# Kernel tuning notes

Hardware: AMD Instinct MI355X
Metric: run time of the kernel (lower is better)

## Reference

```python
import jax, jax.numpy as jnp
import numpy as np

DIM = 512
HEADS = 8
WIN = 10      # window_size
SHIFT = 5     # shift_size
FRAMES = 1000 # num_frames (N)
HIDDEN = 4 * DIM
EPS = 1e-5


def _layernorm(x, w, b):
    m = jnp.mean(x, axis=-1, keepdims=True)
    v = jnp.mean((x - m) ** 2, axis=-1, keepdims=True)
    return (x - m) * jax.lax.rsqrt(v + EPS) * w + b


def _shift_mask(N):
    pos = jnp.arange(N)
    seg = (pos >= N - WIN).astype(jnp.float32) + (pos >= N - SHIFT).astype(jnp.float32)
    seg = seg.reshape(N // WIN, WIN)
    diff = seg[:, :, None] - seg[:, None, :]
    return jnp.where(diff != 0, -100.0, 0.0)


def setup_inputs() -> dict:
    key = jax.random.key(0)
    ks = jax.random.split(key, 16)
    std = 0.02
    inp = {
        "x": jax.random.normal(ks[0], (64, FRAMES, DIM), dtype=jnp.float32),
        "norm1_w": jnp.ones((DIM,), jnp.float32),
        "norm1_b": jnp.zeros((DIM,), jnp.float32),
        "qkv_w": jax.random.normal(ks[1], (3 * DIM, DIM), jnp.float32) * std,
        "qkv_b": jnp.zeros((3 * DIM,), jnp.float32),
        "rel_bias_table": jax.random.normal(ks[2], (2 * WIN - 1, HEADS), jnp.float32) * std,
        "proj_w": jax.random.normal(ks[3], (DIM, DIM), jnp.float32) * std,
        "proj_b": jnp.zeros((DIM,), jnp.float32),
        "norm2_w": jnp.ones((DIM,), jnp.float32),
        "norm2_b": jnp.zeros((DIM,), jnp.float32),
        "fc1_w": jax.random.normal(ks[4], (HIDDEN, DIM), jnp.float32) * std,
        "fc1_b": jnp.zeros((HIDDEN,), jnp.float32),
        "fc2_w": jax.random.normal(ks[5], (DIM, HIDDEN), jnp.float32) * std,
        "fc2_b": jnp.zeros((DIM,), jnp.float32),
    }
    return inp


def reference(x, norm1_w, norm1_b, qkv_w, qkv_b, rel_bias_table, proj_w, proj_b,
              norm2_w, norm2_b, fc1_w, fc1_b, fc2_w, fc2_b):
    B, N, C = x.shape
    hd = C // HEADS
    scale = hd ** -0.5
    nW = N // WIN

    shortcut = x
    h = _layernorm(x, norm1_w, norm1_b)
    h = jnp.roll(h, -SHIFT, axis=1)                      # cyclic shift
    xw = h.reshape(B * nW, WIN, C)                       # window partition

    qkv = xw @ qkv_w.T + qkv_b
    qkv = qkv.reshape(B * nW, WIN, 3, HEADS, hd).transpose(2, 0, 3, 1, 4)
    q, k, v = qkv[0] * scale, qkv[1], qkv[2]

    attn = jnp.einsum('bhqd,bhkd->bhqk', q, k)
    idx = jnp.arange(WIN)[:, None] - jnp.arange(WIN)[None, :] + WIN - 1
    bias = rel_bias_table[idx]
    attn = attn + bias.transpose(2, 0, 1)[None]

    mask = _shift_mask(N)
    attn = attn.reshape(B, nW, HEADS, WIN, WIN) + mask[None, :, None]
    attn = jax.nn.softmax(attn, axis=-1).reshape(B * nW, HEADS, WIN, WIN)

    out = jnp.einsum('bhqk,bhkd->bhqd', attn, v)
    out = out.transpose(0, 2, 1, 3).reshape(B * nW, WIN, C)
    out = out @ proj_w.T + proj_b

    out = out.reshape(B, N, C)                           # window reverse
    out = jnp.roll(out, SHIFT, axis=1)                   # reverse shift

    x = shortcut + out
    h2 = _layernorm(x, norm2_w, norm2_b)
    h2 = jax.nn.gelu(h2 @ fc1_w.T + fc1_b, approximate=False)
    h2 = h2 @ fc2_w.T + fc2_b
    return x + h2
```

## Files before the change

### kernel.cpp

```cpp
#include <hip/hip_runtime.h>

#define DIMC 512
#define HEADS 8
#define HD 64
#define WINS 10
#define SHIFT_SZ 5
#define FRAMES 1000
#define NWIN 100
#define BATCH 64
#define TOKENS 64000
#define HIDDEN 2048

typedef unsigned short u16;
typedef __attribute__((ext_vector_type(8))) short bf16x8;
typedef __attribute__((ext_vector_type(4))) float f32x4;

__device__ __forceinline__ float bf2f(u16 u) { return __uint_as_float(((unsigned)u) << 16); }
__device__ __forceinline__ u16 f2bf(float f) {
    unsigned u = __float_as_uint(f);
    u += 0x7fffu + ((u >> 16) & 1u);
    return (u16)(u >> 16);
}

__global__ __launch_bounds__(256) void cvt_kernel(const float* __restrict__ src,
                                                  u16* __restrict__ dst, int n) {
    const int i = (blockIdx.x * 256 + threadIdx.x) * 4;
    if (i < n) {
        const float4 v = *(const float4*)(src + i);
        *(ushort4*)(dst + i) = make_ushort4(f2bf(v.x), f2bf(v.y), f2bf(v.z), f2bf(v.w));
    }
}

template <int SH>
__global__ __launch_bounds__(256) void ln_kernel(const float* __restrict__ x,
                                                 const float* __restrict__ w,
                                                 const float* __restrict__ b,
                                                 u16* __restrict__ out,
                                                 u16* __restrict__ xb) {
    const int wave = threadIdx.x >> 6, lane = threadIdx.x & 63;
    const int row = blockIdx.x * 4 + wave;
    const float4* rp = (const float4*)(x + (size_t)row * DIMC);
    const float4 v0 = rp[lane];
    const float4 v1 = rp[64 + lane];
    float f[8] = {v0.x, v0.y, v0.z, v0.w, v1.x, v1.y, v1.z, v1.w};
    float sum = 0.f, sq = 0.f;
#pragma unroll
    for (int i = 0; i < 8; i++) { sum += f[i]; sq += f[i] * f[i]; }
#pragma unroll
    for (int off = 32; off >= 1; off >>= 1) {
        sum += __shfl_xor(sum, off);
        sq += __shfl_xor(sq, off);
    }
    const float mean = sum * (1.f / DIMC);
    const float var = sq * (1.f / DIMC) - mean * mean;
    const float rstd = rsqrtf(var + 1e-5f);

    if (xb) {
        u16* xp = xb + (size_t)row * DIMC;
        *(ushort4*)(xp + 4 * lane) = make_ushort4(f2bf(f[0]), f2bf(f[1]), f2bf(f[2]), f2bf(f[3]));
        *(ushort4*)(xp + 256 + 4 * lane) = make_ushort4(f2bf(f[4]), f2bf(f[5]), f2bf(f[6]), f2bf(f[7]));
    }

    const float4 w0 = ((const float4*)w)[lane], w1 = ((const float4*)w)[64 + lane];
    const float4 b0 = ((const float4*)b)[lane], b1 = ((const float4*)b)[64 + lane];
    const float wf[8] = {w0.x, w0.y, w0.z, w0.w, w1.x, w1.y, w1.z, w1.w};
    const float bf[8] = {b0.x, b0.y, b0.z, b0.w, b1.x, b1.y, b1.z, b1.w};
    u16 o[8];
#pragma unroll
    for (int i = 0; i < 8; i++) o[i] = f2bf((f[i] - mean) * rstd * wf[i] + bf[i]);

    int dst = row;
    if (SH) {
        int bb = row / FRAMES;
        int t = row - bb * FRAMES;
        int td = t - SH; if (td < 0) td += FRAMES;
        dst = bb * FRAMES + td;
    }
    u16* op = out + (size_t)dst * DIMC;
    *(ushort4*)(op + 4 * lane) = make_ushort4(o[0], o[1], o[2], o[3]);
    *(ushort4*)(op + 256 + 4 * lane) = make_ushort4(o[4], o[5], o[6], o[7]);
}

__global__ __launch_bounds__(256) void ln_kernel_bf(const u16* __restrict__ x,
                                                    const float* __restrict__ w,
                                                    const float* __restrict__ b,
                                                    u16* __restrict__ out) {
    const int wave = threadIdx.x >> 6, lane = threadIdx.x & 63;
    const int row = blockIdx.x * 4 + wave;
    const uint4 v = ((const uint4*)(x + (size_t)row * DIMC))[lane];
    const unsigned uv[4] = {v.x, v.y, v.z, v.w};
    float f[8];
    float sum = 0.f, sq = 0.f;
#pragma unroll
    for (int i = 0; i < 4; i++) {
        float a = __uint_as_float(uv[i] << 16);
        float c = __uint_as_float(uv[i] & 0xffff0000u);
        f[2 * i] = a; f[2 * i + 1] = c;
        sum += a + c; sq += a * a + c * c;
    }
#pragma unroll
    for (int off = 32; off >= 1; off >>= 1) {
        sum += __shfl_xor(sum, off);
        sq += __shfl_xor(sq, off);
    }
    const float mean = sum * (1.f / DIMC);
    const float var = sq * (1.f / DIMC) - mean * mean;
    const float rstd = rsqrtf(var + 1e-5f);

    const float4 w0 = ((const float4*)w)[2 * lane], w1 = ((const float4*)w)[2 * lane + 1];
    const float4 b0 = ((const float4*)b)[2 * lane], b1 = ((const float4*)b)[2 * lane + 1];
    const float wf[8] = {w0.x, w0.y, w0.z, w0.w, w1.x, w1.y, w1.z, w1.w};
    const float bf[8] = {b0.x, b0.y, b0.z, b0.w, b1.x, b1.y, b1.z, b1.w};
    u16 o[8];
#pragma unroll
    for (int i = 0; i < 8; i++) o[i] = f2bf((f[i] - mean) * rstd * wf[i] + bf[i]);
    uint4 ov;
    ov.x = (unsigned)o[0] | ((unsigned)o[1] << 16);
    ov.y = (unsigned)o[2] | ((unsigned)o[3] << 16);
    ov.z = (unsigned)o[4] | ((unsigned)o[5] << 16);
    ov.w = (unsigned)o[6] | ((unsigned)o[7] << 16);
    ((uint4*)(out + (size_t)row * DIMC))[lane] = ov;
}

#define GLD16(gp, lp)                                                                     \
    __builtin_amdgcn_global_load_lds((const __attribute__((address_space(1))) void*)(gp), \
                                     (__attribute__((address_space(3))) void*)(lp), 16, 0, 0)

template <int MODE>
__global__ __launch_bounds__(256, 2) void gemm_bt(const u16* __restrict__ A,
                                                  const u16* __restrict__ W,
                                                  const float* __restrict__ bias,
                                                  u16* __restrict__ Cb,
                                                  float* __restrict__ Cf,
                                                  const u16* __restrict__ Rb,
                                                  int Nn, int K, int nbn) {
    __shared__ __align__(16) u16 smem[36864];
    const int tid = threadIdx.x;
    const int w = tid >> 6, l = tid & 63;

    const int nwg = gridDim.x;
    const int q8 = nwg >> 3, r8 = nwg & 7;
    const int xcd = blockIdx.x & 7, bidx = blockIdx.x >> 3;
    const int swz = (xcd < r8 ? xcd * (q8 + 1) : r8 * (q8 + 1) + (xcd - r8) * q8) + bidx;
    const int bm = swz / nbn, bn = swz - bm * nbn;

    const int wr = w >> 1, wc = w & 1;
    const int lrow = l & 15, lq = l >> 4;

    f32x4 acc[8][4];
#pragma unroll
    for (int m = 0; m < 8; m++)
#pragma unroll
        for (int n = 0; n < 4; n++) acc[m][n] = (f32x4)0.0f;

    const int gsrc8 = (((tid & 3) ^ ((tid >> 3) & 3)) << 3);
    const u16* Ag = A + (size_t)(bm * 256 + (tid >> 2)) * K + gsrc8;
    const u16* Bg = W + (size_t)(bn * 128 + (tid >> 2)) * K + gsrc8;
    const size_t rowoff = (size_t)64 * K;
    const int lb = w * 512;

#define STAGE(buf, kt) do {                                       \
        u16* sb_ = smem + (buf) * 12288;                          \
        GLD16(Ag + (kt), sb_ + lb);                               \
        GLD16(Ag + rowoff + (kt), sb_ + 2048 + lb);               \
        GLD16(Ag + 2 * rowoff + (kt), sb_ + 4096 + lb);           \
        GLD16(Ag + 3 * rowoff + (kt), sb_ + 6144 + lb);           \
        GLD16(Bg + (kt), sb_ + 8192 + lb);                        \
        GLD16(Bg + rowoff + (kt), sb_ + 10240 + lb);              \
    } while (0)

    const int gran = ((lq ^ ((lrow >> 1) & 3)) << 3);
    const int arow = (wr * 128 + lrow) * 32 + gran;
    const int brow = 8192 + (wc * 64 + lrow) * 32 + gran;

#define COMPUTE(buf) do {                                                          \
        const u16* sb = smem + (buf) * 12288;                                      \
        bf16x8 bv[4];                                                              \
        _Pragma("unroll")                                                          \
        for (int n = 0; n < 4; n++) bv[n] = *(const bf16x8*)(sb + brow + n * 512); \
        _Pragma("unroll")                                                          \
        for (int m = 0; m < 8; m++) {                                              \
            const bf16x8 af = *(const bf16x8*)(sb + arow + m * 512);               \
            _Pragma("unroll")                                                      \
            for (int n = 0; n < 4; n++)              \
                acc[m][n] = __builtin_amdgcn_mfma_f32_16x16x32_bf16(bv[n], af, acc[m][n], 0, 0, 0); \
        }                                                                          \
    } while (0)

    const int nt = K >> 5;
    STAGE(0, 0);
    STAGE(1, 32);
    int cb = 0;
    for (int t = 0; t < nt - 1; ++t) {
        asm volatile("s_waitcnt vmcnt(6)" ::: "memory");
        __builtin_amdgcn_s_barrier();
        __builtin_amdgcn_sched_barrier(0);
        COMPUTE(cb);
        if (t + 2 < nt) {
            const int sbuf = cb == 0 ? 2 : cb - 1;
            STAGE(sbuf, (t + 2) * 32);
        }
        cb = cb == 2 ? 0 : cb + 1;
    }
    asm volatile("s_waitcnt vmcnt(0)" ::: "memory");
    __builtin_amdgcn_s_barrier();
    __builtin_amdgcn_sched_barrier(0);
    COMPUTE(cb);

    if (MODE == 0 || MODE == 1 || MODE == 2) {
        __syncthreads();
#pragma unroll
        for (int m = 0; m < 8; m++) {
            const int row = wr * 128 + m * 16 + lrow;
            const int sw = (row & 7) << 3;
#pragma unroll
            for (int n = 0; n < 4; n++) {
                const int col = wc * 64 + n * 16 + lq * 4;
                const float4 b4 = *(const float4*)(bias + bn * 128 + col);
                float v0 = acc[m][n][0] + b4.x, v1 = acc[m][n][1] + b4.y;
                float v2 = acc[m][n][2] + b4.z, v3 = acc[m][n][3] + b4.w;
                if (MODE == 2) {
                    const float g0 = v0 * (0.7978845608f + 0.0356774081f * v0 * v0);
                    const float g1 = v1 * (0.7978845608f + 0.0356774081f * v1 * v1);
                    const float g2 = v2 * (0.7978845608f + 0.0356774081f * v2 * v2);
                    const float g3 = v3 * (0.7978845608f + 0.0356774081f * v3 * v3);
                    v0 /= (1.f + __expf(-2.f * g0)); v1 /= (1.f + __expf(-2.f * g1));
                    v2 /= (1.f + __expf(-2.f * g2)); v3 /= (1.f + __expf(-2.f * g3));
                }
                *(ushort4*)(smem + row * 128 + ((col ^ sw))) =
                    make_ushort4(f2bf(v0), f2bf(v1), f2bf(v2), f2bf(v3));
            }
        }
        __syncthreads();
        const int c8 = lrow * 8;
#pragma unroll
        for (int i = 0; i < 16; i++) {
            const int r = w * 64 + i * 4 + lq;
            const uint4 val = *(const uint4*)(smem + r * 128 + (c8 ^ ((r & 7) << 3)));
            const int grow = bm * 256 + r;
            if (MODE == 1) {
                int bb = grow / FRAMES;
                int tr = grow - bb * FRAMES;
                int td = tr + SHIFT_SZ; if (td >= FRAMES) td -= FRAMES;
                const size_t dr = (size_t)(bb * FRAMES + td) * DIMC + bn * 128 + c8;
                const uint4 rv = *(const uint4*)(Rb + dr);
                const u16* vp = (const u16*)&val;
                const u16* rp2 = (const u16*)&rv;
                u16 o[8];
#pragma unroll
                for (int k = 0; k < 8; k++) o[k] = f2bf(bf2f(vp[k]) + bf2f(rp2[k]));
                uint4 ov;
                ov.x = (unsigned)o[0] | ((unsigned)o[1] << 16);
                ov.y = (unsigned)o[2] | ((unsigned)o[3] << 16);
                ov.z = (unsigned)o[4] | ((unsigned)o[5] << 16);
                ov.w = (unsigned)o[6] | ((unsigned)o[7] << 16);
                *(uint4*)(Cb + dr) = ov;
            } else {
                *(uint4*)(Cb + (size_t)grow * Nn + bn * 128 + c8) = val;
            }
        }
    } else {
#pragma unroll
        for (int m = 0; m < 8; m++) {
            const int grow = bm * 256 + wr * 128 + m * 16 + lrow;
#pragma unroll
            for (int n = 0; n < 4; n++) {
                const int gcb = bn * 128 + wc * 64 + n * 16 + lq * 4;
                const float4 b4 = *(const float4*)(bias + gcb);
                const size_t dr = (size_t)grow * Nn + gcb;
                const ushort4 rb = *(const ushort4*)(Rb + dr);
                float4 o;
                o.x = acc[m][n][0] + b4.x + bf2f(rb.x);
                o.y = acc[m][n][1] + b4.y + bf2f(rb.y);
                o.z = acc[m][n][2] + b4.z + bf2f(rb.z);
                o.w = acc[m][n][3] + b4.w + bf2f(rb.w);
                *(float4*)(Cf + dr) = o;
            }
        }
    }
#undef COMPUTE
#undef STAGE
}

__global__ __launch_bounds__(256) void attn_kernel(const u16* __restrict__ qkv_c,
                                                   const float* __restrict__ relb,
                                                   u16* __restrict__ out,
                                                   int win0) {
    __shared__ __align__(16) u16 kv[WINS * 3 * DIMC];
    __shared__ float S[HEADS][WINS][WINS];
    const int tid = threadIdx.x;
    const int win = win0 + blockIdx.x;
    const u16* src = qkv_c + (size_t)blockIdx.x * (WINS * 3 * DIMC);
    for (int idx = tid * 8; idx < WINS * 3 * DIMC; idx += 2048)
        *(uint4*)(kv + idx) = *(const uint4*)(src + idx);
    __syncthreads();

    const bool lastw = (win % NWIN) == (NWIN - 1);
    for (int e = tid; e < HEADS * WINS * WINS; e += 256) {
        const int hh = e / (WINS * WINS);
        const int rem = e - hh * WINS * WINS;
        const int i = rem / WINS, j = rem - (rem / WINS) * WINS;
        const u16* qp = kv + i * (3 * DIMC) + hh * HD;
        const u16* kp = kv + j * (3 * DIMC) + DIMC + hh * HD;
        float s = 0.f;
#pragma unroll
        for (int c = 0; c < 64; c++) s += bf2f(qp[c]) * bf2f(kp[c]);
        s *= 0.125f;
        s += relb[(i - j + WINS - 1) * HEADS + hh];
        if (lastw && ((i < SHIFT_SZ) != (j < SHIFT_SZ))) s -= 100.f;
        S[hh][i][j] = s;
    }
    __syncthreads();

    if (tid < HEADS * WINS) {
        const int hh = tid / WINS, i = tid - (tid / WINS) * WINS;
        float m = -1e30f;
#pragma unroll
        for (int j = 0; j < WINS; j++) m = fmaxf(m, S[hh][i][j]);
        float e[WINS], sum = 0.f;
#pragma unroll
        for (int j = 0; j < WINS; j++) { e[j] = __expf(S[hh][i][j] - m); sum += e[j]; }
        const float inv = 1.f / sum;
#pragma unroll
        for (int j = 0; j < WINS; j++) S[hh][i][j] = e[j] * inv;
    }
    __syncthreads();

    {
        const int hh = tid >> 5, dl = tid & 31;
#pragma unroll
        for (int half = 0; half < 2; half++) {
            const int d = dl + half * 32;
            float vv[WINS];
#pragma unroll
            for (int j = 0; j < WINS; j++) vv[j] = bf2f(kv[j * (3 * DIMC) + 2 * DIMC + hh * HD + d]);
#pragma unroll
            for (int i = 0; i < WINS; i++) {
                float o = 0.f;
#pragma unroll
                for (int j = 0; j < WINS; j++) o += S[hh][i][j] * vv[j];
                out[(size_t)(win * WINS + i) * DIMC + hh * HD + d] = f2bf(o);
            }
        }
    }
}

extern "C" void kernel_launch(void* const* d_in, const int* in_sizes, int n_in,
                              void* d_out, int out_size, void* d_ws, size_t ws_size,
                              hipStream_t stream) {
    const float* x     = (const float*)d_in[0];
    const float* n1w   = (const float*)d_in[1];
    const float* n1b   = (const float*)d_in[2];
    const float* qkvw  = (const float*)d_in[3];
    const float* qkvb  = (const float*)d_in[4];
    const float* relb  = (const float*)d_in[5];
    const float* projw = (const float*)d_in[6];
    const float* projb = (const float*)d_in[7];
    const float* n2w   = (const float*)d_in[8];
    const float* n2b   = (const float*)d_in[9];
    const float* fc1w  = (const float*)d_in[10];
    const float* fc1b  = (const float*)d_in[11];
    const float* fc2w  = (const float*)d_in[12];
    const float* fc2b  = (const float*)d_in[13];

    float* outp = (float*)d_out;
    char* ws = (char*)d_ws;
    u16* wb_qkv  = (u16*)(ws);
    u16* wb_proj = (u16*)(ws + 1572864);
    u16* wb_fc1  = (u16*)(ws + 2097152);
    u16* wb_fc2  = (u16*)(ws + 4194304);
    u16* r0  = (u16*)(ws + 6291456);
    u16* xb  = (u16*)(ws + 71827456);
    u16* x2b = (u16*)(ws + 137363456);
    u16* big = (u16*)(ws + 202899456);

    cvt_kernel<<<768, 256, 0, stream>>>(qkvw, wb_qkv, 786432);
    cvt_kernel<<<256, 256, 0, stream>>>(projw, wb_proj, 262144);
    cvt_kernel<<<1024, 256, 0, stream>>>(fc1w, wb_fc1, 1048576);
    cvt_kernel<<<1024, 256, 0, stream>>>(fc2w, wb_fc2, 1048576);

    const size_t avail = ws_size > (size_t)202899456 ? ws_size - (size_t)202899456 : 0;
    const int nc1 = (avail >= (size_t)98304000) ? 2
                  : (avail >= (size_t)39321600) ? 5 : (avail >= (size_t)19660800) ? 10 : 50;
    const int nc2 = (avail >= (size_t)131072000) ? 2
                  : (avail >= (size_t)52428800) ? 5 : (avail >= (size_t)26214400) ? 10 : 25;

    ln_kernel<SHIFT_SZ><<<TOKENS / 4, 256, 0, stream>>>(x, n1w, n1b, r0, xb);

    const int rows1 = TOKENS / nc1;
    for (int c = 0; c < nc1; ++c) {
        const int row0 = c * rows1;
        gemm_bt<0><<<(rows1 / 256) * 12, 256, 0, stream>>>(
            r0 + (size_t)row0 * DIMC, wb_qkv, qkvb, big, nullptr, nullptr, 1536, DIMC, 12);
        attn_kernel<<<rows1 / WINS, 256, 0, stream>>>(big, relb, r0, row0 / WINS);
    }

    gemm_bt<1><<<(TOKENS / 256) * 4, 256, 0, stream>>>(
        r0, wb_proj, projb, x2b, nullptr, xb, DIMC, DIMC, 4);

    ln_kernel_bf<<<TOKENS / 4, 256, 0, stream>>>(x2b, n2w, n2b, r0);

    const int rows2 = TOKENS / nc2;
    for (int c = 0; c < nc2; ++c) {
        const int row0 = c * rows2;
        gemm_bt<2><<<(rows2 / 256) * 16, 256, 0, stream>>>(
            r0 + (size_t)row0 * DIMC, wb_fc1, fc1b, big, nullptr, nullptr, HIDDEN, DIMC, 16);
        gemm_bt<3><<<(rows2 / 256) * 4, 256, 0, stream>>>(
            big, wb_fc2, fc2b, nullptr, outp + (size_t)row0 * DIMC,
            x2b + (size_t)row0 * DIMC, DIMC, HIDDEN, 4);
    }
}
```

Before: 780.1 us.

## Add 256x256-tile 512-thread GEMM for QKV and FC1, issue prefetch before compute

Adds a new gemm_w kernel with 512 threads and 256x256 output tiles, using XCD-aware block swizzling and a two-half epilogue through shared memory. The QKV and FC1 projections switch to it, so each block reads twice as much of the weight matrix per A tile and fewer A re-reads are needed. In the existing GEMM loop, the next stage's global loads are now issued before the MFMA compute instead of after, to overlap memory with math. The larger tile needs 96KB of LDS and more registers per block, which may limit occupancy.

```diff
diff --git a/kernel.cpp b/kernel.cpp
--- a/kernel.cpp
+++ b/kernel.cpp
@@ -182,7 +182,7 @@
         for (int m = 0; m < 8; m++) {                                              \
             const bf16x8 af = *(const bf16x8*)(sb + arow + m * 512);               \
             _Pragma("unroll")                                                      \
-            for (int n = 0; n < 4; n++)              \
+            for (int n = 0; n < 4; n++)                                            \
                 acc[m][n] = __builtin_amdgcn_mfma_f32_16x16x32_bf16(bv[n], af, acc[m][n], 0, 0, 0); \
         }                                                                          \
     } while (0)
@@ -195,11 +195,11 @@
         asm volatile("s_waitcnt vmcnt(6)" ::: "memory");
         __builtin_amdgcn_s_barrier();
         __builtin_amdgcn_sched_barrier(0);
-        COMPUTE(cb);
         if (t + 2 < nt) {
             const int sbuf = cb == 0 ? 2 : cb - 1;
             STAGE(sbuf, (t + 2) * 32);
         }
+        COMPUTE(cb);
         cb = cb == 2 ? 0 : cb + 1;
     }
     asm volatile("s_waitcnt vmcnt(0)" ::: "memory");
@@ -207,7 +207,7 @@
     __builtin_amdgcn_sched_barrier(0);
     COMPUTE(cb);
 
-    if (MODE == 0 || MODE == 1 || MODE == 2) {
+    if (MODE == 1) {
         __syncthreads();
 #pragma unroll
         for (int m = 0; m < 8; m++) {
@@ -217,18 +217,9 @@
             for (int n = 0; n < 4; n++) {
                 const int col = wc * 64 + n * 16 + lq * 4;
                 const float4 b4 = *(const float4*)(bias + bn * 128 + col);
-                float v0 = acc[m][n][0] + b4.x, v1 = acc[m][n][1] + b4.y;
-                float v2 = acc[m][n][2] + b4.z, v3 = acc[m][n][3] + b4.w;
-                if (MODE == 2) {
-                    const float g0 = v0 * (0.7978845608f + 0.0356774081f * v0 * v0);
-                    const float g1 = v1 * (0.7978845608f + 0.0356774081f * v1 * v1);
-                    const float g2 = v2 * (0.7978845608f + 0.0356774081f * v2 * v2);
-                    const float g3 = v3 * (0.7978845608f + 0.0356774081f * v3 * v3);
-                    v0 /= (1.f + __expf(-2.f * g0)); v1 /= (1.f + __expf(-2.f * g1));
-                    v2 /= (1.f + __expf(-2.f * g2)); v3 /= (1.f + __expf(-2.f * g3));
-                }
-                *(ushort4*)(smem + row * 128 + ((col ^ sw))) =
-                    make_ushort4(f2bf(v0), f2bf(v1), f2bf(v2), f2bf(v3));
+                *(ushort4*)(smem + row * 128 + (col ^ sw)) =
+                    make_ushort4(f2bf(acc[m][n][0] + b4.x), f2bf(acc[m][n][1] + b4.y),
+                                 f2bf(acc[m][n][2] + b4.z), f2bf(acc[m][n][3] + b4.w));
             }
         }
         __syncthreads();
@@ -238,26 +229,22 @@
             const int r = w * 64 + i * 4 + lq;
             const uint4 val = *(const uint4*)(smem + r * 128 + (c8 ^ ((r & 7) << 3)));
             const int grow = bm * 256 + r;
-            if (MODE == 1) {
-                int bb = grow / FRAMES;
-                int tr = grow - bb * FRAMES;
-                int td = tr + SHIFT_SZ; if (td >= FRAMES) td -= FRAMES;
-                const size_t dr = (size_t)(bb * FRAMES + td) * DIMC + bn * 128 + c8;
-                const uint4 rv = *(const uint4*)(Rb + dr);
-                const u16* vp = (const u16*)&val;
-                const u16* rp2 = (const u16*)&rv;
-                u16 o[8];
-#pragma unroll
-                for (int k = 0; k < 8; k++) o[k] = f2bf(bf2f(vp[k]) + bf2f(rp2[k]));
-                uint4 ov;
-                ov.x = (unsigned)o[0] | ((unsigned)o[1] << 16);
-                ov.y = (unsigned)o[2] | ((unsigned)o[3] << 16);
-                ov.z = (unsigned)o[4] | ((unsigned)o[5] << 16);
-                ov.w = (unsigned)o[6] | ((unsigned)o[7] << 16);
-                *(uint4*)(Cb + dr) = ov;
-            } else {
-                *(uint4*)(Cb + (size_t)grow * Nn + bn * 128 + c8) = val;
-            }
+            int bb = grow / FRAMES;
+            int tr = grow - bb * FRAMES;
+            int td = tr + SHIFT_SZ; if (td >= FRAMES) td -= FRAMES;
+            const size_t dr = (size_t)(bb * FRAMES + td) * DIMC + bn * 128 + c8;
+            const uint4 rv = *(const uint4*)(Rb + dr);
+            const u16* vp = (const u16*)&val;
+            const u16* rp2 = (const u16*)&rv;
+            u16 o[8];
+#pragma unroll
+            for (int k = 0; k < 8; k++) o[k] = f2bf(bf2f(vp[k]) + bf2f(rp2[k]));
+            uint4 ov;
+            ov.x = (unsigned)o[0] | ((unsigned)o[1] << 16);
+            ov.y = (unsigned)o[2] | ((unsigned)o[3] << 16);
+            ov.z = (unsigned)o[4] | ((unsigned)o[5] << 16);
+            ov.w = (unsigned)o[6] | ((unsigned)o[7] << 16);
+            *(uint4*)(Cb + dr) = ov;
         }
     } else {
 #pragma unroll
@@ -280,6 +267,126 @@
     }
 #undef COMPUTE
 #undef STAGE
+}
+
+template <int MODE>
+__global__ __launch_bounds__(512, 2) void gemm_w(const u16* __restrict__ A,
+                                                 const u16* __restrict__ W,
+                                                 const float* __restrict__ bias,
+                                                 u16* __restrict__ Cb,
+                                                 int Nn, int K, int nbn) {
+    __shared__ __align__(16) u16 smem[49152];
+    const int tid = threadIdx.x;
+    const int w = tid >> 6, l = tid & 63;
+
+    const int nwg = gridDim.x;
+    const int q8 = nwg >> 3, r8 = nwg & 7;
+    const int xcd = blockIdx.x & 7, bidx = blockIdx.x >> 3;
+    const int swz = (xcd < r8 ? xcd * (q8 + 1) : r8 * (q8 + 1) + (xcd - r8) * q8) + bidx;
+    const int bm = swz / nbn, bn = swz - bm * nbn;
+
+    const int wm = w >> 2, wn = w & 3;
+    const int lrow = l & 15, lq = l >> 4;
+
+    f32x4 acc[8][4];
+#pragma unroll
+    for (int m = 0; m < 8; m++)
+#pragma unroll
+        for (int n = 0; n < 4; n++) acc[m][n] = (f32x4)0.0f;
+
+    const int gsrc8 = (((tid & 3) ^ ((tid >> 3) & 3)) << 3);
+    const u16* Ag = A + (size_t)(bm * 256 + (tid >> 2)) * K + gsrc8;
+    const u16* Wg = W + (size_t)(bn * 256 + (tid >> 2)) * K + gsrc8;
+    const size_t roff = (size_t)128 * K;
+    const int lb = w * 512;
+
+#define STAGEW(buf, kt) do {                                      \
+        u16* sb_ = smem + (buf) * 16384;                          \
+        GLD16(Ag + (kt), sb_ + lb);                               \
+        GLD16(Ag + roff + (kt), sb_ + 4096 + lb);                 \
+        GLD16(Wg + (kt), sb_ + 8192 + lb);                        \
+        GLD16(Wg + roff + (kt), sb_ + 12288 + lb);                \
+    } while (0)
+
+    const int gran = ((lq ^ ((lrow >> 1) & 3)) << 3);
+    const int arow = (wm * 128 + lrow) * 32 + gran;
+    const int brow = 8192 + (wn * 64 + lrow) * 32 + gran;
+
+#define COMPUTEW(buf) do {                                                         \
+        const u16* sb = smem + (buf) * 16384;                                      \
+        bf16x8 bv[4];                                                              \
+        _Pragma("unroll")                                                          \
+        for (int n = 0; n < 4; n++) bv[n] = *(const bf16x8*)(sb + brow + n * 512); \
+        _Pragma("unroll")                                                          \
+        for (int m = 0; m < 8; m++) {                                              \
+            const bf16x8 af = *(const bf16x8*)(sb + arow + m * 512);               \
+            _Pragma("unroll")                                                      \
+            for (int n = 0; n < 4; n++)                                            \
+                acc[m][n] = __builtin_amdgcn_mfma_f32_16x16x32_bf16(bv[n], af, acc[m][n], 0, 0, 0); \
+        }                                                                          \
+    } while (0)
+
+    const int nt = K >> 5;
+    STAGEW(0, 0);
+    STAGEW(1, 32);
+    int cb = 0;
+    for (int t = 0; t < nt - 1; ++t) {
+        asm volatile("s_waitcnt vmcnt(4)" ::: "memory");
+        __builtin_amdgcn_s_barrier();
+        __builtin_amdgcn_sched_barrier(0);
+        if (t + 2 < nt) {
+            const int sbuf = cb == 0 ? 2 : cb - 1;
+            STAGEW(sbuf, (t + 2) * 32);
+        }
+        COMPUTEW(cb);
+        cb = cb == 2 ? 0 : cb + 1;
+    }
+    asm volatile("s_waitcnt vmcnt(0)" ::: "memory");
+    __builtin_amdgcn_s_barrier();
+    __builtin_amdgcn_sched_barrier(0);
+    COMPUTEW(cb);
+
+#pragma unroll
+    for (int half = 0; half < 2; half++) {
+        __syncthreads();
+        if (wm == half) {
+#pragma unroll
+            for (int m = 0; m < 8; m++) {
+                const int row = m * 16 + lrow;
+                const int sw = (row & 7) << 3;
+#pragma unroll
+                for (int n = 0; n < 4; n++) {
+                    const int col = wn * 64 + n * 16 + lq * 4;
+                    const float4 b4 = *(const float4*)(bias + bn * 256 + col);
+                    float v0 = acc[m][n][0] + b4.x, v1 = acc[m][n][1] + b4.y;
+                    float v2 = acc[m][n][2] + b4.z, v3 = acc[m][n][3] + b4.w;
+                    if (MODE == 2) {
+                        const float g0 = v0 * (0.7978845608f + 0.0356774081f * v0 * v0);
+                        const float g1 = v1 * (0.7978845608f + 0.0356774081f * v1 * v1);
+                        const float g2 = v2 * (0.7978845608f + 0.0356774081f * v2 * v2);
+                        const float g3 = v3 * (0.7978845608f + 0.0356774081f * v3 * v3);
+                        v0 /= (1.f + __expf(-2.f * g0)); v1 /= (1.f + __expf(-2.f * g1));
+                        v2 /= (1.f + __expf(-2.f * g2)); v3 /= (1.f + __expf(-2.f * g3));
+                    }
+                    const int cidx = (((col & 127) ^ sw)) | (col & 128);
+                    *(ushort4*)(smem + row * 256 + cidx) =
+                        make_ushort4(f2bf(v0), f2bf(v1), f2bf(v2), f2bf(v3));
+                }
+            }
+        }
+        __syncthreads();
+#pragma unroll
+        for (int i = 0; i < 8; i++) {
+            const int r = i * 16 + (tid >> 5);
+            const int c0 = (tid & 31) << 3;
+            const int sw = (r & 7) << 3;
+            const int cA = ((c0 & 127) ^ sw) | (c0 & 128);
+            const uint4 val = *(const uint4*)(smem + r * 256 + cA);
+            *(uint4*)(Cb + (size_t)(bm * 256 + half * 128 + r) * Nn + bn * 256 + c0) = val;
+        }
+    }
+#undef COMPUTEW
+#undef STAGEW
 }
 
 __global__ __launch_bounds__(256) void attn_kernel(const u16* __restrict__ qkv_c,
@@ -390,8 +497,8 @@
     const int rows1 = TOKENS / nc1;
     for (int c = 0; c < nc1; ++c) {
         const int row0 = c * rows1;
-        gemm_bt<0><<<(rows1 / 256) * 12, 256, 0, stream>>>(
-            r0 + (size_t)row0 * DIMC, wb_qkv, qkvb, big, nullptr, nullptr, 1536, DIMC, 12);
+        gemm_w<0><<<(rows1 / 256) * 6, 512, 0, stream>>>(
+            r0 + (size_t)row0 * DIMC, wb_qkv, qkvb, big, 1536, DIMC, 6);
         attn_kernel<<<rows1 / WINS, 256, 0, stream>>>(big, relb, r0, row0 / WINS);
     }
 
@@ -403,8 +510,8 @@
     const int rows2 = TOKENS / nc2;
     for (int c = 0; c < nc2; ++c) {
         const int row0 = c * rows2;
-        gemm_bt<2><<<(rows2 / 256) * 16, 256, 0, stream>>>(
-            r0 + (size_t)row0 * DIMC, wb_fc1, fc1b, big, nullptr, nullptr, HIDDEN, DIMC, 16);
+        gemm_w<2><<<(rows2 / 256) * 8, 512, 0, stream>>>(
+            r0 + (size_t)row0 * DIMC, wb_fc1, fc1b, big, HIDDEN, DIMC, 8);
         gemm_bt<3><<<(rows2 / 256) * 4, 256, 0, stream>>>(
             big, wb_fc2, fc2b, nullptr, outp + (size_t)row0 * DIMC,
             x2b + (size_t)row0 * DIMC, DIMC, HIDDEN, 4);
```

Result: slower. 819.0 us (+5.0%).
